# Kernel optimization log

Hardware: AMD Instinct MI355X
Metric: run time of the kernel (lower is better)

Reference implementation:

```python
import jax, jax.numpy as jnp
import numpy as np

B, L, D, H = 4, 2048, 1024, 16
HD = D // H  # head_dim = 64


def setup_inputs() -> dict:
    key = jax.random.key(0)
    ks = jax.random.split(key, 12)
    s = 1.0 / np.sqrt(D)
    return {
        "Q": jax.random.normal(ks[0], (B, L, D), jnp.float32),
        "K": jax.random.normal(ks[1], (B, L, D), jnp.float32),
        "V": jax.random.normal(ks[2], (B, L, D), jnp.float32),
        "mask": jnp.ones((1, 1, L, L), dtype=bool),
        "Wq_w": jax.random.normal(ks[3], (D, D), jnp.float32) * s,
        "Wq_b": jnp.zeros((D,), jnp.float32),
        "Wk_w": jax.random.normal(ks[4], (D, D), jnp.float32) * s,
        "Wk_b": jnp.zeros((D,), jnp.float32),
        "Wv_w": jax.random.normal(ks[5], (D, D), jnp.float32) * s,
        "Wv_b": jnp.zeros((D,), jnp.float32),
        "out_w": jax.random.normal(ks[6], (D, D), jnp.float32) * s,
        "out_b": jnp.zeros((D,), jnp.float32),
    }


def _split_heads(x):
    b, l, _ = x.shape
    return x.reshape(b, l, H, HD).transpose(0, 2, 1, 3)  # [B,H,L,HD]


def reference(Q, K, V, mask, Wq_w, Wq_b, Wk_w, Wk_b, Wv_w, Wv_b, out_w, out_b):
    # torch Linear: y = x @ W.T + b
    q = _split_heads(Q @ Wq_w.T + Wq_b)
    k = _split_heads(K @ Wk_w.T + Wk_b)
    v = _split_heads(V @ Wv_w.T + Wv_b)
    scores = jnp.einsum("bhqd,bhkd->bhqk", q, k) / jnp.sqrt(jnp.float32(HD))
    scores = jnp.where(mask, scores, -jnp.inf)
    w = jax.nn.softmax(scores, axis=-1)
    o = jnp.einsum("bhqk,bhkd->bhqd", w, v)  # [B,H,L,HD]
    o = o.transpose(0, 2, 1, 3).reshape(Q.shape[0], -1, H * HD)
    return o @ out_w.T + out_b
```

## Files before the change

### kernel.cpp

```cpp
#include <hip/hip_runtime.h>


typedef __attribute__((ext_vector_type(8))) short short8;
typedef __attribute__((ext_vector_type(4))) float f32x4;
typedef unsigned short u16_t;

#define B_SZ 4
#define L_SZ 2048
#define D_SZ 1024
#define H_SZ 16
#define HD_SZ 64
#define M_SZ (B_SZ * L_SZ)
#define K_SZ 1024

__device__ __forceinline__ u16_t f2bf(float x) {
  union { float f; unsigned u; } v; v.f = x;
  unsigned r = v.u + 0x7fffu + ((v.u >> 16) & 1u);
  return (u16_t)(r >> 16);
}

__device__ __forceinline__ void gload16(const void* g, void* l) {
  __builtin_amdgcn_global_load_lds(
      (const __attribute__((address_space(1))) unsigned*)g,
      (__attribute__((address_space(3))) unsigned*)l, 16, 0, 0);
}

__device__ __forceinline__ f32x4 mfma16(short8 a, short8 b, f32x4 c) {
  return __builtin_amdgcn_mfma_f32_16x16x32_bf16(a, b, c, 0, 0, 0);
}

__global__ void convert_w(const float* __restrict__ w0, const float* __restrict__ w1,
                          const float* __restrict__ w2, const float* __restrict__ w3,
                          u16_t* __restrict__ dst) {
  int idx = blockIdx.x * 256 + threadIdx.x;
  int which = idx >> 17;
  int rem = idx & 131071;
  const float* src = (which == 0) ? w0 : (which == 1) ? w1 : (which == 2) ? w2 : w3;
  src += (size_t)rem * 8;
  float4 f0 = *(const float4*)src;
  float4 f1 = *(const float4*)(src + 4);
  short8 u;
  u[0] = (short)f2bf(f0.x); u[1] = (short)f2bf(f0.y);
  u[2] = (short)f2bf(f0.z); u[3] = (short)f2bf(f0.w);
  u[4] = (short)f2bf(f1.x); u[5] = (short)f2bf(f1.y);
  u[6] = (short)f2bf(f1.z); u[7] = (short)f2bf(f1.w);
  *(short8*)(dst + (size_t)idx * 8) = u;
}

template<int APATH, int EPI>
__global__ __launch_bounds__(256, 2)
void gemm_k(const void* __restrict__ Av, const u16_t* __restrict__ Bw,
            const float* __restrict__ bias, void* __restrict__ Cout) {
  __shared__ alignas(16) u16_t lA[128 * 64];
  __shared__ alignas(16) u16_t lB[128 * 64];
  const int tid = threadIdx.x;
  const int l = tid & 63, w = tid >> 6;
  const int wr = w >> 1, wc = w & 1;
  const int m0 = blockIdx.y * 128, n0 = blockIdx.x * 128;

  float bv[4];
#pragma unroll
  for (int nf = 0; nf < 4; ++nf) bv[nf] = bias[n0 + wc * 64 + nf * 16 + (l & 15)];

  f32x4 acc[4][4];
#pragma unroll
  for (int a = 0; a < 4; ++a)
#pragma unroll
    for (int b = 0; b < 4; ++b) { f32x4 z = {0.f, 0.f, 0.f, 0.f}; acc[a][b] = z; }

  for (int kt = 0; kt < K_SZ / 64; ++kt) {
    const int k0 = kt * 64;
#pragma unroll
    for (int it = 0; it < 4; ++it) {
      int c = it * 256 + tid;
      int row = c >> 3, cb = (c & 7) << 4;
      int kb = (cb ^ ((row & 7) << 4)) >> 1;
      gload16(Bw + (size_t)(n0 + row) * K_SZ + k0 + kb, (char*)lB + c * 16);
    }
    if (APATH == 1) {
      const u16_t* Ab = (const u16_t*)Av;
#pragma unroll
      for (int it = 0; it < 4; ++it) {
        int c = it * 256 + tid;
        int row = c >> 3, cb = (c & 7) << 4;
        int kb = (cb ^ ((row & 7) << 4)) >> 1;
        gload16(Ab + (size_t)(m0 + row) * K_SZ + k0 + kb, (char*)lA + c * 16);
      }
    } else {
      const float* Af = (const float*)Av;
#pragma unroll
      for (int it = 0; it < 4; ++it) {
        int c = it * 256 + tid;
        int row = c >> 3, cb = (c & 7) << 4;
        int kb = (cb ^ ((row & 7) << 4)) >> 1;
        const float* src = Af + (size_t)(m0 + row) * K_SZ + k0 + kb;
        float4 f0 = *(const float4*)src;
        float4 f1 = *(const float4*)(src + 4);
        short8 u;
        u[0] = (short)f2bf(f0.x); u[1] = (short)f2bf(f0.y);
        u[2] = (short)f2bf(f0.z); u[3] = (short)f2bf(f0.w);
        u[4] = (short)f2bf(f1.x); u[5] = (short)f2bf(f1.y);
        u[6] = (short)f2bf(f1.z); u[7] = (short)f2bf(f1.w);
        *(short8*)((char*)lA + c * 16) = u;
      }
    }
    __syncthreads();
#pragma unroll
    for (int ksb = 0; ksb < 2; ++ksb) {
      const int colB = ksb * 64 + ((l >> 4) << 4);
      short8 af[4], bfr[4];
#pragma unroll
      for (int mf = 0; mf < 4; ++mf) {
        int row = wr * 64 + mf * 16 + (l & 15);
        af[mf] = *(const short8*)((const char*)lA + row * 128 + (colB ^ ((row & 7) << 4)));
      }
#pragma unroll
      for (int nf = 0; nf < 4; ++nf) {
        int row = wc * 64 + nf * 16 + (l & 15);
        bfr[nf] = *(const short8*)((const char*)lB + row * 128 + (colB ^ ((row & 7) << 4)));
      }
#pragma unroll
      for (int mf = 0; mf < 4; ++mf)
#pragma unroll
        for (int nf = 0; nf < 4; ++nf)
          acc[mf][nf] = mfma16(af[mf], bfr[nf], acc[mf][nf]);
    }
    __syncthreads();
  }
#pragma unroll
  for (int mf = 0; mf < 4; ++mf)
#pragma unroll
    for (int nf = 0; nf < 4; ++nf)
#pragma unroll
      for (int r = 0; r < 4; ++r) {
        int m = m0 + wr * 64 + mf * 16 + ((l >> 4) << 2) + r;
        int n = n0 + wc * 64 + nf * 16 + (l & 15);
        float val = acc[mf][nf][r] + bv[nf];
        if (EPI == 0) {
          u16_t* q = (u16_t*)Cout;
          size_t idx = ((size_t)((m >> 11) * H_SZ + (n >> 6)) * L_SZ + (m & 2047)) * 64 + (n & 63);
          q[idx] = f2bf(val);
        } else if (EPI == 1) {
          u16_t* vt = (u16_t*)Cout;
          size_t idx = ((size_t)((m >> 11) * H_SZ + (n >> 6)) * 64 + (n & 63)) * L_SZ + (m & 2047);
          vt[idx] = f2bf(val);
        } else {
          ((float*)Cout)[(size_t)m * D_SZ + n] = val;
        }
      }
}

__global__ __launch_bounds__(256, 2)
void attn_k(const u16_t* __restrict__ qbuf, const u16_t* __restrict__ kbuf,
            const u16_t* __restrict__ vtbuf, u16_t* __restrict__ obuf) {
  __shared__ alignas(16) u16_t lK[64 * 64];
  __shared__ alignas(16) u16_t lV[64 * 64];
  __shared__ alignas(16) u16_t lP[4][16 * 64];
  const int tid = threadIdx.x;
  const int l = tid & 63, w = tid >> 6;
  const int b = blockIdx.z, h = blockIdx.y, qb0 = blockIdx.x;
  const int bh = b * H_SZ + h;

  const int tok = qb0 * 64 + w * 16 + (l & 15);
  const u16_t* qrow = qbuf + ((size_t)bh * L_SZ + tok) * 64;
  short8 qf0 = *(const short8*)(qrow + ((l >> 4) << 3));
  short8 qf1 = *(const short8*)(qrow + 32 + ((l >> 4) << 3));

  f32x4 oacc[4];
#pragma unroll
  for (int nd = 0; nd < 4; ++nd) { f32x4 z = {0.f, 0.f, 0.f, 0.f}; oacc[nd] = z; }
  float mrun[4] = {-INFINITY, -INFINITY, -INFINITY, -INFINITY};
  float lrun[4] = {0.f, 0.f, 0.f, 0.f};

  const u16_t* kbase = kbuf + (size_t)bh * L_SZ * 64;
  const u16_t* vtbase = vtbuf + (size_t)bh * 64 * L_SZ;
  const int colB0 = (l >> 4) << 4;

  for (int kt = 0; kt < L_SZ / 64; ++kt) {
    const u16_t* ks_ = kbase + kt * 64 * 64;
    const u16_t* vs_ = vtbase + kt * 64;
#pragma unroll
    for (int it = 0; it < 2; ++it) {
      int c = it * 256 + tid;
      int row = c >> 3, cb = (c & 7) << 4;
      int kb = (cb ^ ((row & 7) << 4)) >> 1;
      gload16(ks_ + row * 64 + kb, (char*)lK + c * 16);
      gload16(vs_ + (size_t)row * L_SZ + kb, (char*)lV + c * 16);
    }
    __syncthreads();

    f32x4 s[4];
#pragma unroll
    for (int nf = 0; nf < 4; ++nf) {
      int rk = nf * 16 + (l & 15);
      const char* kr = (const char*)lK + rk * 128;
      short8 k0 = *(const short8*)(kr + (colB0 ^ ((rk & 7) << 4)));
      short8 k1 = *(const short8*)(kr + ((64 + colB0) ^ ((rk & 7) << 4)));
      f32x4 z = {0.f, 0.f, 0.f, 0.f};
      z = mfma16(qf0, k0, z);
      s[nf] = mfma16(qf1, k1, z);
    }
#pragma unroll
    for (int nf = 0; nf < 4; ++nf)
#pragma unroll
      for (int r = 0; r < 4; ++r) s[nf][r] *= 0.125f;

    float pm[4], sf[4], rs[4];
#pragma unroll
    for (int r = 0; r < 4; ++r) {
      pm[r] = fmaxf(fmaxf(s[0][r], s[1][r]), fmaxf(s[2][r], s[3][r]));
#pragma unroll
      for (int d = 1; d < 16; d <<= 1) pm[r] = fmaxf(pm[r], __shfl_xor(pm[r], d));
      float mn = fmaxf(mrun[r], pm[r]);
      sf[r] = __expf(mrun[r] - mn);
      mrun[r] = mn;
      rs[r] = 0.f;
    }
#pragma unroll
    for (int nf = 0; nf < 4; ++nf)
#pragma unroll
      for (int r = 0; r < 4; ++r) {
        float p = __expf(s[nf][r] - mrun[r]);
        s[nf][r] = p;
        rs[r] += p;
      }
#pragma unroll
    for (int r = 0; r < 4; ++r) {
#pragma unroll
      for (int d = 1; d < 16; d <<= 1) rs[r] += __shfl_xor(rs[r], d);
      lrun[r] = lrun[r] * sf[r] + rs[r];
    }
#pragma unroll
    for (int nd = 0; nd < 4; ++nd)
#pragma unroll
      for (int r = 0; r < 4; ++r) oacc[nd][r] *= sf[r];

    u16_t* wp = lP[w];
#pragma unroll
    for (int nf = 0; nf < 4; ++nf)
#pragma unroll
      for (int r = 0; r < 4; ++r) {
        int prow = ((l >> 4) << 2) + r;
        int pcb = (nf * 16 + (l & 15)) * 2;
        *(u16_t*)((char*)wp + prow * 128 + (pcb ^ ((prow & 7) << 4))) = f2bf(s[nf][r]);
      }
#pragma unroll
    for (int ksb = 0; ksb < 2; ++ksb) {
      int colB = ksb * 64 + colB0;
      int prow = l & 15;
      short8 pa = *(const short8*)((const char*)wp + prow * 128 + (colB ^ ((prow & 7) << 4)));
#pragma unroll
      for (int nd = 0; nd < 4; ++nd) {
        int rv = nd * 16 + (l & 15);
        short8 vf = *(const short8*)((const char*)lV + rv * 128 + (colB ^ ((rv & 7) << 4)));
        oacc[nd] = mfma16(pa, vf, oacc[nd]);
      }
    }
    __syncthreads();
  }
#pragma unroll
  for (int nd = 0; nd < 4; ++nd)
#pragma unroll
    for (int r = 0; r < 4; ++r) {
      int t2 = qb0 * 64 + w * 16 + ((l >> 4) << 2) + r;
      float ov = oacc[nd][r] / lrun[r];
      obuf[((size_t)b * L_SZ + t2) * D_SZ + h * 64 + nd * 16 + (l & 15)] = f2bf(ov);
    }
}

extern "C" void kernel_launch(void* const* d_in, const int* in_sizes, int n_in,
                              void* d_out, int out_size, void* d_ws, size_t ws_size,
                              hipStream_t stream) {
  const float* Q   = (const float*)d_in[0];
  const float* Kin = (const float*)d_in[1];
  const float* V   = (const float*)d_in[2];
  const float* Wq  = (const float*)d_in[4];
  const float* Wqb = (const float*)d_in[5];
  const float* Wk  = (const float*)d_in[6];
  const float* Wkb = (const float*)d_in[7];
  const float* Wv  = (const float*)d_in[8];
  const float* Wvb = (const float*)d_in[9];
  const float* Wo  = (const float*)d_in[10];
  const float* Wob = (const float*)d_in[11];

  char* ws = (char*)d_ws;
  const size_t MB = 1ull << 20;
  u16_t* Wqbf = (u16_t*)(ws + 0 * MB);
  u16_t* Wkbf = (u16_t*)(ws + 2 * MB);
  u16_t* Wvbf = (u16_t*)(ws + 4 * MB);
  u16_t* Wobf = (u16_t*)(ws + 6 * MB);
  u16_t* qb   = (u16_t*)(ws + 8 * MB);
  u16_t* kb   = (u16_t*)(ws + 24 * MB);
  u16_t* vtb  = (u16_t*)(ws + 40 * MB);
  u16_t* ob   = (u16_t*)(ws + 56 * MB);

  convert_w<<<2048, 256, 0, stream>>>(Wq, Wk, Wv, Wo, (u16_t*)ws);

  dim3 gg(D_SZ / 128, M_SZ / 128);
  gemm_k<0, 0><<<gg, 256, 0, stream>>>(Q,   Wqbf, Wqb, qb);
  gemm_k<0, 0><<<gg, 256, 0, stream>>>(Kin, Wkbf, Wkb, kb);
  gemm_k<0, 1><<<gg, 256, 0, stream>>>(V,   Wvbf, Wvb, vtb);

  attn_k<<<dim3(L_SZ / 64, H_SZ, B_SZ), 256, 0, stream>>>(qb, kb, vtb, ob);

  gemm_k<1, 2><<<gg, 256, 0, stream>>>(ob, Wobf, Wob, (float*)d_out);
}
```

Measured before the change: 494.8 us.

## Double-buffer attention K/V, lazy softmax rescale, exp2 with pre-scaled Q, bf16 pre-conversion

Q/K/V activations are converted to bf16 up front in a dedicated kernel, so the GEMMs can load both operands directly into LDS with global_load_lds. The attention loop double-buffers K/V tiles so the next tile loads during compute, with one barrier per iteration instead of two. Softmax now uses exp2 with the 1/sqrt(d)*log2e factor folded into the Q projection epilogue. The running-max rescale is skipped unless the max grows past a threshold, and the row-sum shuffle reduction moves out of the loop to the end. Block-index swizzling for locality across XCDs and s_setprio around the MFMA sections are also added; the cost is an extra full pass over the activations and more LDS per attention block.

```diff
diff --git a/kernel.cpp b/kernel.cpp
--- a/kernel.cpp
+++ b/kernel.cpp
@@ -9,9 +9,11 @@
 #define L_SZ 2048
 #define D_SZ 1024
 #define H_SZ 16
-#define HD_SZ 64
 #define M_SZ (B_SZ * L_SZ)
 #define K_SZ 1024
+
+#define QSCALE 0.18033688011112042f
+#define DEFER_THR 11.54f
 
 __device__ __forceinline__ u16_t f2bf(float x) {
   union { float f; unsigned u; } v; v.f = x;
@@ -19,6 +21,14 @@
   return (u16_t)(r >> 16);
 }
 
+__device__ __forceinline__ float exp2fast(float x) {
+#if __has_builtin(__builtin_amdgcn_exp2f)
+  return __builtin_amdgcn_exp2f(x);
+#else
+  return __exp2f(x);
+#endif
+}
+
 __device__ __forceinline__ void gload16(const void* g, void* l) {
   __builtin_amdgcn_global_load_lds(
       (const __attribute__((address_space(1))) unsigned*)g,
@@ -27,6 +37,17 @@
 
 __device__ __forceinline__ f32x4 mfma16(short8 a, short8 b, f32x4 c) {
   return __builtin_amdgcn_mfma_f32_16x16x32_bf16(a, b, c, 0, 0, 0);
+}
+
+__device__ __forceinline__ void conv8(const float* src, u16_t* dst) {
+  float4 f0 = *(const float4*)src;
+  float4 f1 = *(const float4*)(src + 4);
+  short8 u;
+  u[0] = (short)f2bf(f0.x); u[1] = (short)f2bf(f0.y);
+  u[2] = (short)f2bf(f0.z); u[3] = (short)f2bf(f0.w);
+  u[4] = (short)f2bf(f1.x); u[5] = (short)f2bf(f1.y);
+  u[6] = (short)f2bf(f1.z); u[7] = (short)f2bf(f1.w);
+  *(short8*)dst = u;
 }
 
 __global__ void convert_w(const float* __restrict__ w0, const float* __restrict__ w1,
@@ -36,31 +57,34 @@
   int which = idx >> 17;
   int rem = idx & 131071;
   const float* src = (which == 0) ? w0 : (which == 1) ? w1 : (which == 2) ? w2 : w3;
-  src += (size_t)rem * 8;
-  float4 f0 = *(const float4*)src;
-  float4 f1 = *(const float4*)(src + 4);
-  short8 u;
-  u[0] = (short)f2bf(f0.x); u[1] = (short)f2bf(f0.y);
-  u[2] = (short)f2bf(f0.z); u[3] = (short)f2bf(f0.w);
-  u[4] = (short)f2bf(f1.x); u[5] = (short)f2bf(f1.y);
-  u[6] = (short)f2bf(f1.z); u[7] = (short)f2bf(f1.w);
-  *(short8*)(dst + (size_t)idx * 8) = u;
-}
-
-template<int APATH, int EPI>
+  conv8(src + (size_t)rem * 8, dst + (size_t)idx * 8);
+}
+
+__global__ void convert_a(const float* __restrict__ a0, const float* __restrict__ a1,
+                          const float* __restrict__ a2, u16_t* __restrict__ dst) {
+  int idx = blockIdx.x * 256 + threadIdx.x;
+  int which = idx >> 20;
+  int rem = idx & 1048575;
+  const float* src = (which == 0) ? a0 : (which == 1) ? a1 : a2;
+  conv8(src + (size_t)rem * 8, dst + (size_t)idx * 8);
+}
+
+template<int EPI>
 __global__ __launch_bounds__(256, 2)
-void gemm_k(const void* __restrict__ Av, const u16_t* __restrict__ Bw,
-            const float* __restrict__ bias, void* __restrict__ Cout) {
+void gemm_k(const u16_t* __restrict__ Abf, const u16_t* __restrict__ Bw,
+            const float* __restrict__ bias, void* __restrict__ Cout, float scale) {
   __shared__ alignas(16) u16_t lA[128 * 64];
   __shared__ alignas(16) u16_t lB[128 * 64];
   const int tid = threadIdx.x;
   const int l = tid & 63, w = tid >> 6;
   const int wr = w >> 1, wc = w & 1;
-  const int m0 = blockIdx.y * 128, n0 = blockIdx.x * 128;
-
-  float bv[4];
-#pragma unroll
-  for (int nf = 0; nf < 4; ++nf) bv[nf] = bias[n0 + wc * 64 + nf * 16 + (l & 15)];
+  const int lin = blockIdx.x;
+  const int nw = (lin & 7) * 64 + (lin >> 3);
+  const int m0 = (nw >> 3) * 128, n0 = (nw & 7) * 128;
+
+  float bvs[4];
+#pragma unroll
+  for (int nf = 0; nf < 4; ++nf) bvs[nf] = bias[n0 + wc * 64 + nf * 16 + (l & 15)] * scale;
 
   f32x4 acc[4][4];
 #pragma unroll
@@ -73,36 +97,10 @@
 #pragma unroll
     for (int it = 0; it < 4; ++it) {
       int c = it * 256 + tid;
-      int row = c >> 3, cb = (c & 7) << 4;
-      int kb = (cb ^ ((row & 7) << 4)) >> 1;
+      int row = c >> 3;
+      int kb = ((((c & 7) << 4)) ^ ((row & 7) << 4)) >> 1;
       gload16(Bw + (size_t)(n0 + row) * K_SZ + k0 + kb, (char*)lB + c * 16);
-    }
-    if (APATH == 1) {
-      const u16_t* Ab = (const u16_t*)Av;
-#pragma unroll
-      for (int it = 0; it < 4; ++it) {
-        int c = it * 256 + tid;
-        int row = c >> 3, cb = (c & 7) << 4;
-        int kb = (cb ^ ((row & 7) << 4)) >> 1;
-        gload16(Ab + (size_t)(m0 + row) * K_SZ + k0 + kb, (char*)lA + c * 16);
-      }
-    } else {
-      const float* Af = (const float*)Av;
-#pragma unroll
-      for (int it = 0; it < 4; ++it) {
-        int c = it * 256 + tid;
-        int row = c >> 3, cb = (c & 7) << 4;
-        int kb = (cb ^ ((row & 7) << 4)) >> 1;
-        const float* src = Af + (size_t)(m0 + row) * K_SZ + k0 + kb;
-        float4 f0 = *(const float4*)src;
-        float4 f1 = *(const float4*)(src + 4);
-        short8 u;
-        u[0] = (short)f2bf(f0.x); u[1] = (short)f2bf(f0.y);
-        u[2] = (short)f2bf(f0.z); u[3] = (short)f2bf(f0.w);
-        u[4] = (short)f2bf(f1.x); u[5] = (short)f2bf(f1.y);
-        u[6] = (short)f2bf(f1.z); u[7] = (short)f2bf(f1.w);
-        *(short8*)((char*)lA + c * 16) = u;
-      }
+      gload16(Abf + (size_t)(m0 + row) * K_SZ + k0 + kb, (char*)lA + c * 16);
     }
     __syncthreads();
 #pragma unroll
@@ -135,7 +133,7 @@
       for (int r = 0; r < 4; ++r) {
         int m = m0 + wr * 64 + mf * 16 + ((l >> 4) << 2) + r;
         int n = n0 + wc * 64 + nf * 16 + (l & 15);
-        float val = acc[mf][nf][r] + bv[nf];
+        float val = fmaf(acc[mf][nf][r], scale, bvs[nf]);
         if (EPI == 0) {
           u16_t* q = (u16_t*)Cout;
           size_t idx = ((size_t)((m >> 11) * H_SZ + (n >> 6)) * L_SZ + (m & 2047)) * 64 + (n & 63);
@@ -153,12 +151,14 @@
 __global__ __launch_bounds__(256, 2)
 void attn_k(const u16_t* __restrict__ qbuf, const u16_t* __restrict__ kbuf,
             const u16_t* __restrict__ vtbuf, u16_t* __restrict__ obuf) {
-  __shared__ alignas(16) u16_t lK[64 * 64];
-  __shared__ alignas(16) u16_t lV[64 * 64];
+  __shared__ alignas(16) u16_t lK[2][64 * 64];
+  __shared__ alignas(16) u16_t lV[2][64 * 64];
   __shared__ alignas(16) u16_t lP[4][16 * 64];
   const int tid = threadIdx.x;
   const int l = tid & 63, w = tid >> 6;
-  const int b = blockIdx.z, h = blockIdx.y, qb0 = blockIdx.x;
+  const int lin = blockIdx.x;
+  const int nw = (lin & 7) * 256 + (lin >> 3);
+  const int qb0 = nw & 31, h = (nw >> 5) & 15, b = nw >> 9;
   const int bh = b * H_SZ + h;
 
   const int tok = qb0 * 64 + w * 16 + (l & 15);
@@ -170,80 +170,83 @@
 #pragma unroll
   for (int nd = 0; nd < 4; ++nd) { f32x4 z = {0.f, 0.f, 0.f, 0.f}; oacc[nd] = z; }
   float mrun[4] = {-INFINITY, -INFINITY, -INFINITY, -INFINITY};
-  float lrun[4] = {0.f, 0.f, 0.f, 0.f};
+  float lpart[4] = {0.f, 0.f, 0.f, 0.f};
 
   const u16_t* kbase = kbuf + (size_t)bh * L_SZ * 64;
   const u16_t* vtbase = vtbuf + (size_t)bh * 64 * L_SZ;
   const int colB0 = (l >> 4) << 4;
 
-  for (int kt = 0; kt < L_SZ / 64; ++kt) {
-    const u16_t* ks_ = kbase + kt * 64 * 64;
+  auto STAGE = [&](int buf, int kt) {
+    const u16_t* ks_ = kbase + kt * 4096;
     const u16_t* vs_ = vtbase + kt * 64;
 #pragma unroll
     for (int it = 0; it < 2; ++it) {
       int c = it * 256 + tid;
-      int row = c >> 3, cb = (c & 7) << 4;
-      int kb = (cb ^ ((row & 7) << 4)) >> 1;
-      gload16(ks_ + row * 64 + kb, (char*)lK + c * 16);
-      gload16(vs_ + (size_t)row * L_SZ + kb, (char*)lV + c * 16);
-    }
+      int row = c >> 3;
+      int kb = ((((c & 7) << 4)) ^ ((row & 7) << 4)) >> 1;
+      gload16(ks_ + row * 64 + kb, (char*)lK[buf] + c * 16);
+      gload16(vs_ + (size_t)row * L_SZ + kb, (char*)lV[buf] + c * 16);
+    }
+  };
+
+  STAGE(0, 0);
+  const int NT = L_SZ / 64;
+  for (int kt = 0; kt < NT; ++kt) {
+    const int cur = kt & 1;
     __syncthreads();
+    if (kt + 1 < NT) STAGE(cur ^ 1, kt + 1);
+
+    const char* Kb = (const char*)lK[cur];
+    const char* Vb = (const char*)lV[cur];
 
     f32x4 s[4];
+    __builtin_amdgcn_s_setprio(1);
 #pragma unroll
     for (int nf = 0; nf < 4; ++nf) {
       int rk = nf * 16 + (l & 15);
-      const char* kr = (const char*)lK + rk * 128;
+      const char* kr = Kb + rk * 128;
       short8 k0 = *(const short8*)(kr + (colB0 ^ ((rk & 7) << 4)));
       short8 k1 = *(const short8*)(kr + ((64 + colB0) ^ ((rk & 7) << 4)));
       f32x4 z = {0.f, 0.f, 0.f, 0.f};
       z = mfma16(qf0, k0, z);
       s[nf] = mfma16(qf1, k1, z);
     }
-#pragma unroll
-    for (int nf = 0; nf < 4; ++nf)
-#pragma unroll
-      for (int r = 0; r < 4; ++r) s[nf][r] *= 0.125f;
-
-    float pm[4], sf[4], rs[4];
+    __builtin_amdgcn_s_setprio(0);
+
+    float pm[4];
 #pragma unroll
     for (int r = 0; r < 4; ++r) {
       pm[r] = fmaxf(fmaxf(s[0][r], s[1][r]), fmaxf(s[2][r], s[3][r]));
 #pragma unroll
-      for (int d = 1; d < 16; d <<= 1) pm[r] = fmaxf(pm[r], __shfl_xor(pm[r], d));
-      float mn = fmaxf(mrun[r], pm[r]);
-      sf[r] = __expf(mrun[r] - mn);
-      mrun[r] = mn;
-      rs[r] = 0.f;
-    }
+      for (int d2 = 1; d2 < 16; d2 <<= 1) pm[r] = fmaxf(pm[r], __shfl_xor(pm[r], d2));
+    }
+    int need = (pm[0] > mrun[0] + DEFER_THR) | (pm[1] > mrun[1] + DEFER_THR) |
+               (pm[2] > mrun[2] + DEFER_THR) | (pm[3] > mrun[3] + DEFER_THR);
+    if (__any(need)) {
+#pragma unroll
+      for (int r = 0; r < 4; ++r) {
+        float mn = fmaxf(mrun[r], pm[r]);
+        float sf = exp2fast(mrun[r] - mn);
+        mrun[r] = mn;
+        lpart[r] *= sf;
+#pragma unroll
+        for (int nd = 0; nd < 4; ++nd) oacc[nd][r] *= sf;
+      }
+    }
+    u16_t* wp = lP[w];
 #pragma unroll
     for (int nf = 0; nf < 4; ++nf)
 #pragma unroll
       for (int r = 0; r < 4; ++r) {
-        float p = __expf(s[nf][r] - mrun[r]);
-        s[nf][r] = p;
-        rs[r] += p;
-      }
-#pragma unroll
-    for (int r = 0; r < 4; ++r) {
-#pragma unroll
-      for (int d = 1; d < 16; d <<= 1) rs[r] += __shfl_xor(rs[r], d);
-      lrun[r] = lrun[r] * sf[r] + rs[r];
-    }
-#pragma unroll
-    for (int nd = 0; nd < 4; ++nd)
-#pragma unroll
-      for (int r = 0; r < 4; ++r) oacc[nd][r] *= sf[r];
-
-    u16_t* wp = lP[w];
-#pragma unroll
-    for (int nf = 0; nf < 4; ++nf)
-#pragma unroll
-      for (int r = 0; r < 4; ++r) {
+        float p = exp2fast(s[nf][r] - mrun[r]);
+        lpart[r] += p;
         int prow = ((l >> 4) << 2) + r;
         int pcb = (nf * 16 + (l & 15)) * 2;
-        *(u16_t*)((char*)wp + prow * 128 + (pcb ^ ((prow & 7) << 4))) = f2bf(s[nf][r]);
-      }
+        union { float f; unsigned u; } cv; cv.f = p;
+        *(u16_t*)((char*)wp + prow * 128 + (pcb ^ ((prow & 7) << 4))) =
+            (u16_t)((cv.u + 0x8000u) >> 16);
+      }
+    __builtin_amdgcn_s_setprio(1);
 #pragma unroll
     for (int ksb = 0; ksb < 2; ++ksb) {
       int colB = ksb * 64 + colB0;
@@ -252,19 +255,27 @@
 #pragma unroll
       for (int nd = 0; nd < 4; ++nd) {
         int rv = nd * 16 + (l & 15);
-        short8 vf = *(const short8*)((const char*)lV + rv * 128 + (colB ^ ((rv & 7) << 4)));
+        short8 vf = *(const short8*)(Vb + rv * 128 + (colB ^ ((rv & 7) << 4)));
         oacc[nd] = mfma16(pa, vf, oacc[nd]);
       }
     }
-    __syncthreads();
+    __builtin_amdgcn_s_setprio(0);
+  }
+  float lr[4];
+#pragma unroll
+  for (int r = 0; r < 4; ++r) {
+    lr[r] = lpart[r];
+#pragma unroll
+    for (int d2 = 1; d2 < 16; d2 <<= 1) lr[r] += __shfl_xor(lr[r], d2);
+    lr[r] = 1.0f / lr[r];
   }
 #pragma unroll
   for (int nd = 0; nd < 4; ++nd)
 #pragma unroll
     for (int r = 0; r < 4; ++r) {
       int t2 = qb0 * 64 + w * 16 + ((l >> 4) << 2) + r;
-      float ov = oacc[nd][r] / lrun[r];
-      obuf[((size_t)b * L_SZ + t2) * D_SZ + h * 64 + nd * 16 + (l & 15)] = f2bf(ov);
+      obuf[((size_t)b * L_SZ + t2) * D_SZ + h * 64 + nd * 16 + (l & 15)] =
+          f2bf(oacc[nd][r] * lr[r]);
     }
 }
 
@@ -289,19 +300,23 @@
   u16_t* Wkbf = (u16_t*)(ws + 2 * MB);
   u16_t* Wvbf = (u16_t*)(ws + 4 * MB);
   u16_t* Wobf = (u16_t*)(ws + 6 * MB);
-  u16_t* qb   = (u16_t*)(ws + 8 * MB);
-  u16_t* kb   = (u16_t*)(ws + 24 * MB);
-  u16_t* vtb  = (u16_t*)(ws + 40 * MB);
-  u16_t* ob   = (u16_t*)(ws + 56 * MB);
+  u16_t* Abf  = (u16_t*)(ws + 8 * MB);
+  u16_t* Qbf  = Abf;
+  u16_t* Kbf  = (u16_t*)(ws + 24 * MB);
+  u16_t* Vbf  = (u16_t*)(ws + 40 * MB);
+  u16_t* qb   = (u16_t*)(ws + 56 * MB);
+  u16_t* kb   = (u16_t*)(ws + 8 * MB);
+  u16_t* vtb  = (u16_t*)(ws + 24 * MB);
+  u16_t* ob   = (u16_t*)(ws + 40 * MB);
 
   convert_w<<<2048, 256, 0, stream>>>(Wq, Wk, Wv, Wo, (u16_t*)ws);
-
-  dim3 gg(D_SZ / 128, M_SZ / 128);
-  gemm_k<0, 0><<<gg, 256, 0, stream>>>(Q,   Wqbf, Wqb, qb);
-  gemm_k<0, 0><<<gg, 256, 0, stream>>>(Kin, Wkbf, Wkb, kb);
-  gemm_k<0, 1><<<gg, 256, 0, stream>>>(V,   Wvbf, Wvb, vtb);
-
-  attn_k<<<dim3(L_SZ / 64, H_SZ, B_SZ), 256, 0, stream>>>(qb, kb, vtb, ob);
-
-  gemm_k<1, 2><<<gg, 256, 0, stream>>>(ob, Wobf, Wob, (float*)d_out);
-}
+  convert_a<<<12288, 256, 0, stream>>>(Q, Kin, V, Abf);
+
+  gemm_k<0><<<512, 256, 0, stream>>>(Qbf, Wqbf, Wqb, qb, QSCALE);
+  gemm_k<0><<<512, 256, 0, stream>>>(Kbf, Wkbf, Wkb, kb, 1.0f);
+  gemm_k<1><<<512, 256, 0, stream>>>(Vbf, Wvbf, Wvb, vtb, 1.0f);
+
+  attn_k<<<2048, 256, 0, stream>>>(qb, kb, vtb, ob);
+
+  gemm_k<2><<<512, 256, 0, stream>>>(ob, Wobf, Wob, (float*)d_out, 1.0f);
+}
```

Result: faster. 409.3 us (-17.3%).
